# Optimization experiments

Hardware: AMD Instinct MI355X
Metric: run time of the kernel (lower is better)

The kernel has to match this reference:

```python
import jax, jax.numpy as jnp
import numpy as np
from jax.scipy.special import logsumexp

B, T, D, H, K = 32, 512, 768, 256, 32


def setup_inputs() -> dict:
    key = jax.random.key(0)
    ks = jax.random.split(key, 12)
    x = jax.random.normal(ks[0], (B, T, D), jnp.float32)
    lengths = jax.random.randint(ks[1], (B,), T // 2, T + 1).astype(jnp.int32)
    mask = jnp.arange(T)[None, :] < lengths[:, None]  # [B,T] bool
    targets = jax.random.randint(ks[2], (B, T), 0, K)

    def p(k, shape, fan):
        return jax.random.normal(k, shape, jnp.float32) / np.sqrt(fan).astype(np.float32)

    W_ih_f = p(ks[3], (4 * H, D), D); W_hh_f = p(ks[4], (4 * H, H), H)
    W_ih_b = p(ks[5], (4 * H, D), D); W_hh_b = p(ks[6], (4 * H, H), H)
    b_f = jnp.zeros((4 * H,), jnp.float32); b_b = jnp.zeros((4 * H,), jnp.float32)
    W_clf = p(ks[7], (K, 2 * H), 2 * H); b_clf = jnp.zeros((K,), jnp.float32)
    start_t = jax.random.uniform(ks[8], (K,), jnp.float32, -0.1, 0.1)
    end_t = jax.random.uniform(ks[9], (K,), jnp.float32, -0.1, 0.1)
    trans = jax.random.uniform(ks[10], (K, K), jnp.float32, -0.1, 0.1)
    return {"input": x, "lengths": lengths, "mask": mask, "targets": targets,
            "W_ih_f": W_ih_f, "W_hh_f": W_hh_f, "b_f": b_f,
            "W_ih_b": W_ih_b, "W_hh_b": W_hh_b, "b_b": b_b,
            "W_clf": W_clf, "b_clf": b_clf,
            "start_t": start_t, "end_t": end_t, "trans": trans}


def _lstm_dir(x_tbd, W_ih, W_hh, b):
    # x_tbd: [T,B,D] -> hs [T,B,H], torch gate order (i,f,g,o)
    Hh = W_hh.shape[1]
    pre = jnp.einsum('tbd,gd->tbg', x_tbd, W_ih) + b  # precompute input projections

    def step(carry, p_t):
        h, c = carry
        g = p_t + h @ W_hh.T
        i, f, gg, o = jnp.split(g, 4, axis=-1)
        c = jax.nn.sigmoid(f) * c + jax.nn.sigmoid(i) * jnp.tanh(gg)
        h = jax.nn.sigmoid(o) * jnp.tanh(c)
        return (h, c), h

    b_sz = x_tbd.shape[1]
    init = (jnp.zeros((b_sz, Hh), x_tbd.dtype), jnp.zeros((b_sz, Hh), x_tbd.dtype))
    _, hs = jax.lax.scan(step, init, pre)
    return hs


def _emissions(x, lengths, W_ih_f, W_hh_f, b_f, W_ih_b, W_hh_b, b_b, W_clf, b_clf):
    Tn = x.shape[1]
    t_idx = jnp.arange(Tn)[None, :]
    # per-sequence reversal of the valid prefix (emulates packed bidirectional LSTM)
    rev_idx = jnp.where(t_idx < lengths[:, None], lengths[:, None] - 1 - t_idx, t_idx)
    h_f = _lstm_dir(x.transpose(1, 0, 2), W_ih_f, W_hh_f, b_f).transpose(1, 0, 2)
    x_rev = jnp.take_along_axis(x, rev_idx[:, :, None], axis=1)
    h_b = _lstm_dir(x_rev.transpose(1, 0, 2), W_ih_b, W_hh_b, b_b).transpose(1, 0, 2)
    h_b = jnp.take_along_axis(h_b, rev_idx[:, :, None], axis=1)  # un-flip
    hcat = jnp.concatenate([h_f, h_b], axis=-1)  # [B,T,2H]
    return hcat @ W_clf.T + b_clf  # [B,T,K]


def _crf_nll(em, targets, mask, lengths, start_t, end_t, trans):
    maskf = mask.astype(em.dtype)
    # numerator (gold path score)
    em_sc = jnp.take_along_axis(em, targets[:, :, None], axis=2)[..., 0]  # [B,T]
    tr_sc = trans[targets[:, :-1], targets[:, 1:]]  # [B,T-1]
    num = start_t[targets[:, 0]] + em_sc[:, 0] + jnp.sum((tr_sc + em_sc[:, 1:]) * maskf[:, 1:], axis=1)
    last_tags = jnp.take_along_axis(targets, (lengths - 1).astype(targets.dtype)[:, None], axis=1)[:, 0]
    num = num + end_t[last_tags]
    # log partition via forward algorithm
    def fwd_step(alpha, inp):
        e_t, m_t = inp
        nxt = logsumexp(alpha[:, :, None] + trans[None] + e_t[:, None, :], axis=1)
        return jnp.where(m_t[:, None], nxt, alpha), None

    alpha0 = start_t[None] + em[:, 0]
    alpha, _ = jax.lax.scan(fwd_step, alpha0, (em[:, 1:].transpose(1, 0, 2), mask[:, 1:].T))
    logZ = logsumexp(alpha + end_t[None], axis=1)
    return -jnp.mean(num - logZ)


def _viterbi(em, mask, start_t, end_t, trans):
    Kn = trans.shape[0]

    def vit_step(score, inp):
        e_t, m_t = inp
        bc = score[:, :, None] + trans[None] + e_t[:, None, :]  # [B,Kprev,Kcur]
        nxt = jnp.max(bc, axis=1)
        idx = jnp.argmax(bc, axis=1)  # [B,K] best previous tag
        idx = jnp.where(m_t[:, None], idx, jnp.arange(Kn)[None, :])  # identity on pads
        return jnp.where(m_t[:, None], nxt, score), idx

    score0 = start_t[None] + em[:, 0]
    score, hist = jax.lax.scan(vit_step, score0, (em[:, 1:].transpose(1, 0, 2), mask[:, 1:].T))
    last = jnp.argmax(score + end_t[None], axis=1)  # [B]

    def back(tag, h):
        prev = jnp.take_along_axis(h, tag[:, None], axis=1)[:, 0]
        return prev, prev

    _, tags_prev = jax.lax.scan(back, last, hist, reverse=True)  # [T-1,B]
    tags = jnp.concatenate([tags_prev, last[None]], axis=0).T  # [B,T]
    return jnp.where(mask, tags, 0)  # zero_pad


def reference(input, lengths, mask, targets, W_ih_f, W_hh_f, b_f, W_ih_b, W_hh_b, b_b,
              W_clf, b_clf, start_t, end_t, trans):
    em = _emissions(input, lengths, W_ih_f, W_hh_f, b_f, W_ih_b, W_hh_b, b_b, W_clf, b_clf)
    loss = _crf_nll(em, targets, mask, lengths, start_t, end_t, trans)
    preds = _viterbi(em, mask, start_t, end_t, trans)
    return loss, preds
```

## Files before the change

### kernel.cpp

```cpp
#include <hip/hip_runtime.h>
#include <hip/hip_bf16.h>


#define NB 32
#define NT 512
#define ND 768
#define NH 256
#define NK 32

__global__ __launch_bounds__(256) void k_sgemm(const float* __restrict__ A,
                                               const float* __restrict__ Wf,
                                               const float* __restrict__ Wb,
                                               float* __restrict__ C) {
    __shared__ float As[2][16][132];
    __shared__ float Bs[2][16][132];
    const int tid = threadIdx.x;
    const int bx = blockIdx.x;
    const int by = blockIdx.y;
    const int tx = tid & 15, ty = tid >> 4;
    const int sm = tid >> 2;
    const int sk = (tid & 3) * 4;
    float acc[8][8];
#pragma unroll
    for (int i = 0; i < 8; ++i)
#pragma unroll
        for (int j = 0; j < 8; ++j) acc[i][j] = 0.f;

    const float* Arow0 = A + (size_t)(by * 128 + sm) * ND + sk;
    const float* Arow1 = A + (size_t)(by * 128 + 64 + sm) * ND + sk;
    const int gn0 = bx * 128 + sm, gn1 = gn0 + 64;
    const float* W0 = (gn0 < 1024) ? (Wf + (size_t)gn0 * ND + sk) : (Wb + (size_t)(gn0 - 1024) * ND + sk);
    const float* W1 = (gn1 < 1024) ? (Wf + (size_t)gn1 * ND + sk) : (Wb + (size_t)(gn1 - 1024) * ND + sk);

    {
        float4 a0 = *(const float4*)(Arow0);
        float4 a1 = *(const float4*)(Arow1);
        float4 w0 = *(const float4*)(W0);
        float4 w1 = *(const float4*)(W1);
        As[0][sk + 0][sm] = a0.x; As[0][sk + 1][sm] = a0.y; As[0][sk + 2][sm] = a0.z; As[0][sk + 3][sm] = a0.w;
        As[0][sk + 0][64 + sm] = a1.x; As[0][sk + 1][64 + sm] = a1.y; As[0][sk + 2][64 + sm] = a1.z; As[0][sk + 3][64 + sm] = a1.w;
        Bs[0][sk + 0][sm] = w0.x; Bs[0][sk + 1][sm] = w0.y; Bs[0][sk + 2][sm] = w0.z; Bs[0][sk + 3][sm] = w0.w;
        Bs[0][sk + 0][64 + sm] = w1.x; Bs[0][sk + 1][64 + sm] = w1.y; Bs[0][sk + 2][64 + sm] = w1.z; Bs[0][sk + 3][64 + sm] = w1.w;
    }
    __syncthreads();

    int cur = 0;
    for (int k0 = 0; k0 < ND; k0 += 16) {
        const bool more = (k0 + 16) < ND;
        float4 na0, na1, nw0, nw1;
        if (more) {
            na0 = *(const float4*)(Arow0 + k0 + 16);
            na1 = *(const float4*)(Arow1 + k0 + 16);
            nw0 = *(const float4*)(W0 + k0 + 16);
            nw1 = *(const float4*)(W1 + k0 + 16);
        }
#pragma unroll
        for (int kk = 0; kk < 16; ++kk) {
            float a[8], b[8];
            *(float4*)&a[0] = *(const float4*)&As[cur][kk][ty * 4];
            *(float4*)&a[4] = *(const float4*)&As[cur][kk][64 + ty * 4];
            *(float4*)&b[0] = *(const float4*)&Bs[cur][kk][tx * 4];
            *(float4*)&b[4] = *(const float4*)&Bs[cur][kk][64 + tx * 4];
#pragma unroll
            for (int i = 0; i < 8; ++i)
#pragma unroll
                for (int j = 0; j < 8; ++j)
                    acc[i][j] = fmaf(a[i], b[j], acc[i][j]);
        }
        if (more) {
            const int nxt = cur ^ 1;
            As[nxt][sk + 0][sm] = na0.x; As[nxt][sk + 1][sm] = na0.y; As[nxt][sk + 2][sm] = na0.z; As[nxt][sk + 3][sm] = na0.w;
            As[nxt][sk + 0][64 + sm] = na1.x; As[nxt][sk + 1][64 + sm] = na1.y; As[nxt][sk + 2][64 + sm] = na1.z; As[nxt][sk + 3][64 + sm] = na1.w;
            Bs[nxt][sk + 0][sm] = nw0.x; Bs[nxt][sk + 1][sm] = nw0.y; Bs[nxt][sk + 2][sm] = nw0.z; Bs[nxt][sk + 3][sm] = nw0.w;
            Bs[nxt][sk + 0][64 + sm] = nw1.x; Bs[nxt][sk + 1][64 + sm] = nw1.y; Bs[nxt][sk + 2][64 + sm] = nw1.z; Bs[nxt][sk + 3][64 + sm] = nw1.w;
            __syncthreads();
            cur = nxt;
        }
    }
#pragma unroll
    for (int i = 0; i < 8; ++i) {
        int m = by * 128 + ((i < 4) ? (ty * 4 + i) : (64 + ty * 4 + (i - 4)));
        float* Crow = C + (size_t)m * 2048 + bx * 128;
        *(float4*)(Crow + tx * 4)      = make_float4(acc[i][0], acc[i][1], acc[i][2], acc[i][3]);
        *(float4*)(Crow + 64 + tx * 4) = make_float4(acc[i][4], acc[i][5], acc[i][6], acc[i][7]);
    }
}

__global__ __launch_bounds__(256) void k_wt4(const float* __restrict__ Whf,
                                             const float* __restrict__ Whb,
                                             float4* __restrict__ Wt4) {
    int gid = blockIdx.x * 256 + threadIdx.x;
    if (gid >= 131072) return;
    int dir = gid >> 16;
    int k   = (gid >> 8) & 255;
    int j   = gid & 255;
    const float* W = dir ? Whb : Whf;
    Wt4[gid] = make_float4(W[(size_t)(0 * 256 + j) * 256 + k],
                           W[(size_t)(1 * 256 + j) * 256 + k],
                           W[(size_t)(2 * 256 + j) * 256 + k],
                           W[(size_t)(3 * 256 + j) * 256 + k]);
}

__device__ __forceinline__ float sigm(float x) { return 1.f / (1.f + expf(-x)); }

__global__ __launch_bounds__(256, 1) void k_lstm4(const float* __restrict__ C,
                                                  const float4* __restrict__ Wt4,
                                                  const float* __restrict__ b_f,
                                                  const float* __restrict__ b_b,
                                                  const int* __restrict__ lengths,
                                                  float* __restrict__ h_f,
                                                  float* __restrict__ h_b) {
    __shared__ float hsh[4][272];
    const int tid = threadIdx.x;
    const int g = blockIdx.x & 63, s = blockIdx.x >> 6;
    const int b = g & 31, dir = g >> 5;
    const int j0 = s * 64;
    const float* bias = dir ? b_b : b_f;
    float* hdir = dir ? h_b : h_f;

    const int j = tid >> 2;
    const int kq = tid & 3;
    const int w = tid >> 6;
    const int lane = tid & 63;

    float4 wreg[64];
    {
        const float4* wb = Wt4 + ((size_t)dir * 256 + kq * 64) * 256 + j0 + j;
#pragma unroll
        for (int i = 0; i < 64; ++i) wreg[i] = wb[(size_t)i * 256];
    }
    float4 breg = make_float4(0.f, 0.f, 0.f, 0.f);
    if (kq == 0)
        breg = make_float4(bias[j0 + j], bias[256 + j0 + j],
                           bias[512 + j0 + j], bias[768 + j0 + j]);
    const int mylen = lengths[b];
    float creg = 0.f;

    for (int t = 0; t < NT; ++t) {
        float4 pre = make_float4(0.f, 0.f, 0.f, 0.f);
        if (kq == 0) {
            int src_t = t;
            if (dir) src_t = (t < mylen) ? (mylen - 1 - t) : t;
            const float* Crow = C + (size_t)(b * 512 + src_t) * 2048 + dir * 1024 + j0 + j;
            pre.x = Crow[0]; pre.y = Crow[256]; pre.z = Crow[512]; pre.w = Crow[768];
        }
        float4 acc = make_float4(0.f, 0.f, 0.f, 0.f);
        if (t > 0) {
            const float* hp = hdir + ((size_t)b * 512 + (t - 1)) * 256 + 4 * lane;
            unsigned long long u0, u1;
            int guard = 0;
            for (;;) {
                u0 = __hip_atomic_load((const unsigned long long*)hp,
                                       __ATOMIC_RELAXED, __HIP_MEMORY_SCOPE_AGENT);
                u1 = __hip_atomic_load((const unsigned long long*)(hp + 2),
                                       __ATOMIC_RELAXED, __HIP_MEMORY_SCOPE_AGENT);
                if ((unsigned)(u0 & 0xFFFFFFFFu) != 0xFFFFFFFFu &&
                    (unsigned)(u0 >> 32)        != 0xFFFFFFFFu &&
                    (unsigned)(u1 & 0xFFFFFFFFu) != 0xFFFFFFFFu &&
                    (unsigned)(u1 >> 32)        != 0xFFFFFFFFu) break;
                if (++guard > (1 << 24)) break;
            }
            const int d0 = 4 * lane;
            float* dst = &hsh[w][(d0 >> 6) * 68 + (d0 & 63)];
            float lo0 = __uint_as_float((unsigned)(u0 & 0xFFFFFFFFu));
            float hi0 = __uint_as_float((unsigned)(u0 >> 32));
            float lo1 = __uint_as_float((unsigned)(u1 & 0xFFFFFFFFu));
            float hi1 = __uint_as_float((unsigned)(u1 >> 32));
            *(float4*)dst = make_float4(lo0, hi0, lo1, hi1);
            asm volatile("s_waitcnt lgkmcnt(0)" ::: "memory");
            __builtin_amdgcn_sched_barrier(0);
            const float* src = &hsh[w][kq * 68];
#pragma unroll
            for (int c = 0; c < 16; ++c) {
                float ha[4];
                *(float4*)ha = *(const float4*)(src + 4 * c);
#pragma unroll
                for (int i = 0; i < 4; ++i) {
                    float4 wv = wreg[c * 4 + i];
                    acc.x = fmaf(wv.x, ha[i], acc.x);
                    acc.y = fmaf(wv.y, ha[i], acc.y);
                    acc.z = fmaf(wv.z, ha[i], acc.z);
                    acc.w = fmaf(wv.w, ha[i], acc.w);
                }
            }
        }
        if (kq == 0) {
            acc.x += pre.x + breg.x; acc.y += pre.y + breg.y;
            acc.z += pre.z + breg.z; acc.w += pre.w + breg.w;
        }
#pragma unroll
        for (int off = 1; off <= 2; off <<= 1) {
            acc.x += __shfl_xor(acc.x, off);
            acc.y += __shfl_xor(acc.y, off);
            acc.z += __shfl_xor(acc.z, off);
            acc.w += __shfl_xor(acc.w, off);
        }
        float ig = sigm(acc.x), fg = sigm(acc.y), gt = tanhf(acc.z), og = sigm(acc.w);
        creg = fg * creg + ig * gt;
        float hn = og * tanhf(creg);
        if (kq == 0)
            __hip_atomic_store(hdir + ((size_t)b * 512 + t) * 256 + j0 + j, hn,
                               __ATOMIC_RELAXED, __HIP_MEMORY_SCOPE_AGENT);
    }
}

__global__ __launch_bounds__(256) void k_em(const float* __restrict__ hf,
                                            const float* __restrict__ hb,
                                            const float* __restrict__ Wclf,
                                            const float* __restrict__ bclf,
                                            const int* __restrict__ lengths,
                                            float* __restrict__ em) {
    extern __shared__ float4 wc4[];
    const int tid = threadIdx.x;
    for (int idx = tid; idx < 4096; idx += 256) {
        int jq = idx >> 5, ko = idx & 31;
        wc4[idx] = *(const float4*)(Wclf + (size_t)ko * 512 + jq * 4);
    }
    __syncthreads();
    const int r = tid >> 5, ko = tid & 31;
    const int m = blockIdx.x * 8 + r;
    const int b = m >> 9, t = m & 511;
    const int len = lengths[b];
    const int rev = (t < len) ? (len - 1 - t) : t;
    const float* hfr = hf + (size_t)m * 256;
    const float* hbr = hb + (size_t)(b * 512 + rev) * 256;
    float acc = bclf[ko];
#pragma unroll 4
    for (int jq = 0; jq < 64; ++jq) {
        float4 h4 = *(const float4*)(hfr + jq * 4);
        float4 ww = wc4[jq * 32 + ko];
        acc += h4.x * ww.x + h4.y * ww.y + h4.z * ww.z + h4.w * ww.w;
    }
#pragma unroll 4
    for (int jq = 0; jq < 64; ++jq) {
        float4 h4 = *(const float4*)(hbr + jq * 4);
        float4 ww = wc4[(64 + jq) * 32 + ko];
        acc += h4.x * ww.x + h4.y * ww.y + h4.z * ww.z + h4.w * ww.w;
    }
    em[(size_t)m * 32 + ko] = acc;
}

__global__ __launch_bounds__(64) void k_crfvit(const float* __restrict__ em,
                                               const int* __restrict__ targets,
                                               const int* __restrict__ lengths,
                                               const float* __restrict__ start_t,
                                               const float* __restrict__ end_t,
                                               const float* __restrict__ trans,
                                               float* __restrict__ numv,
                                               float* __restrict__ logZv,
                                               float* __restrict__ out) {
    __shared__ float trans_s[32][33];
    __shared__ float vec[32];
    __shared__ unsigned char hist[511 * 32];
    const int tid = threadIdx.x;
    const int b = blockIdx.x & 31;
    const int mode = blockIdx.x >> 5;
    for (int idx = tid; idx < 1024; idx += 64) trans_s[idx >> 5][idx & 31] = trans[idx];
    const int len = lengths[b];
    const float* emb = em + (size_t)b * 512 * 32;
    const int k = tid & 31, half = tid >> 5;
    if (tid < 32) vec[tid] = start_t[tid] + emb[tid];
    __syncthreads();

    if (mode == 0) {
        for (int t = 1; t < NT; ++t) {
            bool mv = t < len;
            int kp0 = half * 16;
            float m = -1e30f;
#pragma unroll 4
            for (int i = 0; i < 16; ++i)
                m = fmaxf(m, vec[kp0 + i] + trans_s[kp0 + i][k]);
            float m2 = fmaxf(m, __shfl_xor(m, 32));
            float ssum = 0.f;
#pragma unroll 4
            for (int i = 0; i < 16; ++i)
                ssum += __expf(vec[kp0 + i] + trans_s[kp0 + i][k] - m2);
            ssum += __shfl_xor(ssum, 32);
            float anew = m2 + __logf(ssum) + emb[t * 32 + k];
            __syncthreads();
            if (half == 0 && mv) vec[k] = anew;
            __syncthreads();
        }
        float val = (tid < 32) ? vec[tid] + end_t[tid] : -1e30f;
        float m = val;
#pragma unroll
        for (int off = 32; off >= 1; off >>= 1) m = fmaxf(m, __shfl_xor(m, off));
        float e = (tid < 32) ? __expf(val - m) : 0.f;
#pragma unroll
        for (int off = 32; off >= 1; off >>= 1) e += __shfl_xor(e, off);
        if (tid == 0) logZv[b] = m + __logf(e);
        const int* tg = targets + b * 512;
        float partial = 0.f;
        for (int t = 1 + tid; t < NT; t += 64) {
            if (t < len) {
                int y0 = tg[t - 1], y1 = tg[t];
                partial += trans_s[y0][y1] + emb[t * 32 + y1];
            }
        }
#pragma unroll
        for (int off = 32; off >= 1; off >>= 1) partial += __shfl_xor(partial, off);
        if (tid == 0) {
            int y00 = tg[0];
            int yl = tg[len - 1];
            numv[b] = partial + start_t[y00] + emb[y00] + end_t[yl];
        }
    } else {
        for (int t = 1; t < NT; ++t) {
            bool mv = t < len;
            int kp0 = half * 16;
            float e = emb[t * 32 + k];
            float m = -1e30f; int mi = kp0;
#pragma unroll 4
            for (int i = 0; i < 16; ++i) {
                float v = (vec[kp0 + i] + trans_s[kp0 + i][k]) + e;
                if (v > m) { m = v; mi = kp0 + i; }
            }
            float mo = __shfl_xor(m, 32);
            int io = __shfl_xor(mi, 32);
            float mlow = half ? mo : m;   int ilow = half ? io : mi;
            float mhigh = half ? m : mo;  int ihigh = half ? mi : io;
            float bm; int bi;
            if (mhigh > mlow) { bm = mhigh; bi = ihigh; } else { bm = mlow; bi = ilow; }
            __syncthreads();
            if (half == 0) {
                hist[(t - 1) * 32 + k] = (unsigned char)(mv ? bi : k);
                if (mv) vec[k] = bm;
            }
            __syncthreads();
        }
        float val = (tid < 32) ? vec[tid] + end_t[tid] : -1e30f;
        int idx = (tid < 32) ? tid : 63;
#pragma unroll
        for (int off = 32; off >= 1; off >>= 1) {
            float vo = __shfl_xor(val, off);
            int io = __shfl_xor(idx, off);
            if (vo > val || (vo == val && io < idx)) { val = vo; idx = io; }
        }
        int cur = idx;
        float* ob = out + 1 + (size_t)b * 512;
        if (tid == 0) ob[511] = (511 < len) ? (float)cur : 0.f;
        for (int t2 = 510; t2 >= 0; --t2) {
            cur = hist[t2 * 32 + cur];
            if (tid == 0) ob[t2] = (t2 < len) ? (float)cur : 0.f;
        }
    }
}

__global__ __launch_bounds__(64) void k_loss(const float* __restrict__ numv,
                                             const float* __restrict__ logZv,
                                             float* __restrict__ out) {
    int tid = threadIdx.x;
    float v = (tid < 32) ? (logZv[tid] - numv[tid]) : 0.f;
#pragma unroll
    for (int off = 32; off >= 1; off >>= 1) v += __shfl_xor(v, off);
    if (tid == 0) out[0] = v / 32.f;
}

extern "C" void kernel_launch(void* const* d_in, const int* in_sizes, int n_in,
                              void* d_out, int out_size, void* d_ws, size_t ws_size,
                              hipStream_t stream) {
    const float* x       = (const float*)d_in[0];
    const int*   lengths = (const int*)d_in[1];
    const int*   targets = (const int*)d_in[3];
    const float* W_ih_f  = (const float*)d_in[4];
    const float* W_hh_f  = (const float*)d_in[5];
    const float* b_f     = (const float*)d_in[6];
    const float* W_ih_b  = (const float*)d_in[7];
    const float* W_hh_b  = (const float*)d_in[8];
    const float* b_b     = (const float*)d_in[9];
    const float* W_clf   = (const float*)d_in[10];
    const float* b_clf   = (const float*)d_in[11];
    const float* start_t = (const float*)d_in[12];
    const float* end_t   = (const float*)d_in[13];
    const float* trans   = (const float*)d_in[14];
    float* out = (float*)d_out;
    float* ws = (float*)d_ws;

    float* C     = ws;
    float* h_f   = C + (size_t)16384 * 2048;
    float* h_b   = h_f + (size_t)32 * 512 * 256;
    float* em    = h_b + (size_t)32 * 512 * 256;
    float4* Wt4  = (float4*)(em + (size_t)32 * 512 * 32);
    float* numv  = (float*)(Wt4 + 131072);
    float* logZv = numv + 32;

    hipMemsetAsync(h_f, 0xFF, (size_t)2 * 32 * 512 * 256 * sizeof(float), stream);
    k_wt4<<<512, 256, 0, stream>>>(W_hh_f, W_hh_b, Wt4);
    k_sgemm<<<dim3(16, 128), 256, 0, stream>>>(x, W_ih_f, W_ih_b, C);
    k_lstm4<<<256, 256, 0, stream>>>(C, Wt4, b_f, b_b, lengths, h_f, h_b);
    k_em<<<2048, 256, 65536, stream>>>(h_f, h_b, W_clf, b_clf, lengths, em);
    k_crfvit<<<64, 64, 0, stream>>>(em, targets, lengths, start_t, end_t, trans, numv, logZv, out);
    k_loss<<<1, 64, 0, stream>>>(numv, logZv, out);
}
```

Before: 2.563 ms.

## Split LSTM recurrence across twice as many blocks with weights in registers and LDS

The recurrent LSTM kernel now uses 512 blocks, each owning 32 hidden units instead of 64. Each thread covers a 32-element slice of the hidden-state reduction, with half of its W_hh slice in registers and half in shared memory, so register pressure drops enough for two blocks per CU. The aim is to shorten each block's serial per-step dot product and spread the recurrence over more CUs. In exchange there are twice as many blocks spin-waiting on global hidden-state flags, an extra shuffle stage in the reduction, LDS weight reads on every step, and a hang risk if all 512 spinning blocks are not resident at once.

```diff
diff --git a/kernel.cpp b/kernel.cpp
--- a/kernel.cpp
+++ b/kernel.cpp
@@ -103,46 +103,46 @@
 
 __device__ __forceinline__ float sigm(float x) { return 1.f / (1.f + expf(-x)); }
 
-__global__ __launch_bounds__(256, 1) void k_lstm4(const float* __restrict__ C,
+__global__ __launch_bounds__(256, 2) void k_lstm5(const float* __restrict__ C,
                                                   const float4* __restrict__ Wt4,
                                                   const float* __restrict__ b_f,
                                                   const float* __restrict__ b_b,
                                                   const int* __restrict__ lengths,
                                                   float* __restrict__ h_f,
                                                   float* __restrict__ h_b) {
-    __shared__ float hsh[4][272];
+    __shared__ float4 wlds[16][256];
+    __shared__ float hsh[4][288];
     const int tid = threadIdx.x;
     const int g = blockIdx.x & 63, s = blockIdx.x >> 6;
     const int b = g & 31, dir = g >> 5;
-    const int j0 = s * 64;
+    const int j0 = s * 32;
     const float* bias = dir ? b_b : b_f;
     float* hdir = dir ? h_b : h_f;
 
-    const int j = tid >> 2;
-    const int kq = tid & 3;
+    const int j = tid >> 3;
+    const int kq = tid & 7;
     const int w = tid >> 6;
     const int lane = tid & 63;
 
-    float4 wreg[64];
+    float4 wreg[16];
     {
-        const float4* wb = Wt4 + ((size_t)dir * 256 + kq * 64) * 256 + j0 + j;
-#pragma unroll
-        for (int i = 0; i < 64; ++i) wreg[i] = wb[(size_t)i * 256];
-    }
-    float4 breg = make_float4(0.f, 0.f, 0.f, 0.f);
-    if (kq == 0)
-        breg = make_float4(bias[j0 + j], bias[256 + j0 + j],
-                           bias[512 + j0 + j], bias[768 + j0 + j]);
+        const float4* wb = Wt4 + ((size_t)dir * 256 + 32 * kq) * 256 + j0 + j;
+#pragma unroll
+        for (int u = 0; u < 16; ++u) wreg[u] = wb[(size_t)u * 256];
+#pragma unroll
+        for (int u = 0; u < 16; ++u) wlds[u][tid] = wb[(size_t)(16 + u) * 256];
+    }
+    float preBias = (kq < 4) ? bias[kq * 256 + j0 + j] : 0.f;
     const int mylen = lengths[b];
     float creg = 0.f;
+    __syncthreads();
 
     for (int t = 0; t < NT; ++t) {
-        float4 pre = make_float4(0.f, 0.f, 0.f, 0.f);
-        if (kq == 0) {
+        float preS = 0.f;
+        if (kq < 4) {
             int src_t = t;
             if (dir) src_t = (t < mylen) ? (mylen - 1 - t) : t;
-            const float* Crow = C + (size_t)(b * 512 + src_t) * 2048 + dir * 1024 + j0 + j;
-            pre.x = Crow[0]; pre.y = Crow[256]; pre.z = Crow[512]; pre.w = Crow[768];
+            preS = C[(size_t)(b * 512 + src_t) * 2048 + dir * 1024 + kq * 256 + j0 + j];
         }
         float4 acc = make_float4(0.f, 0.f, 0.f, 0.f);
         if (t > 0) {
@@ -158,22 +158,21 @@
                     (unsigned)(u0 >> 32)        != 0xFFFFFFFFu &&
                     (unsigned)(u1 & 0xFFFFFFFFu) != 0xFFFFFFFFu &&
                     (unsigned)(u1 >> 32)        != 0xFFFFFFFFu) break;
-                if (++guard > (1 << 24)) break;
-            }
-            const int d0 = 4 * lane;
-            float* dst = &hsh[w][(d0 >> 6) * 68 + (d0 & 63)];
-            float lo0 = __uint_as_float((unsigned)(u0 & 0xFFFFFFFFu));
-            float hi0 = __uint_as_float((unsigned)(u0 >> 32));
-            float lo1 = __uint_as_float((unsigned)(u1 & 0xFFFFFFFFu));
-            float hi1 = __uint_as_float((unsigned)(u1 >> 32));
-            *(float4*)dst = make_float4(lo0, hi0, lo1, hi1);
+                if (++guard > (1 << 22)) break;
+            }
+            float* dst = &hsh[w][(lane >> 3) * 36 + ((4 * lane) & 31)];
+            *(float4*)dst = make_float4(
+                __uint_as_float((unsigned)(u0 & 0xFFFFFFFFu)),
+                __uint_as_float((unsigned)(u0 >> 32)),
+                __uint_as_float((unsigned)(u1 & 0xFFFFFFFFu)),
+                __uint_as_float((unsigned)(u1 >> 32)));
             asm volatile("s_waitcnt lgkmcnt(0)" ::: "memory");
             __builtin_amdgcn_sched_barrier(0);
-            const float* src = &hsh[w][kq * 68];
-#pragma unroll
-            for (int c = 0; c < 16; ++c) {
+            const float* hbp = &hsh[w][kq * 36];
+#pragma unroll
+            for (int c = 0; c < 4; ++c) {
                 float ha[4];
-                *(float4*)ha = *(const float4*)(src + 4 * c);
+                *(float4*)ha = *(const float4*)(hbp + 4 * c);
 #pragma unroll
                 for (int i = 0; i < 4; ++i) {
                     float4 wv = wreg[c * 4 + i];
@@ -183,13 +182,27 @@
                     acc.w = fmaf(wv.w, ha[i], acc.w);
                 }
             }
-        }
-        if (kq == 0) {
-            acc.x += pre.x + breg.x; acc.y += pre.y + breg.y;
-            acc.z += pre.z + breg.z; acc.w += pre.w + breg.w;
-        }
-#pragma unroll
-        for (int off = 1; off <= 2; off <<= 1) {
+#pragma unroll
+            for (int c = 0; c < 4; ++c) {
+                float ha[4];
+                *(float4*)ha = *(const float4*)(hbp + 16 + 4 * c);
+#pragma unroll
+                for (int i = 0; i < 4; ++i) {
+                    float4 wv = wlds[c * 4 + i][tid];
+                    acc.x = fmaf(wv.x, ha[i], acc.x);
+                    acc.y = fmaf(wv.y, ha[i], acc.y);
+                    acc.z = fmaf(wv.z, ha[i], acc.z);
+                    acc.w = fmaf(wv.w, ha[i], acc.w);
+                }
+            }
+        }
+        float add = preS + preBias;
+        acc.x += (kq == 0) ? add : 0.f;
+        acc.y += (kq == 1) ? add : 0.f;
+        acc.z += (kq == 2) ? add : 0.f;
+        acc.w += (kq == 3) ? add : 0.f;
+#pragma unroll
+        for (int off = 1; off <= 4; off <<= 1) {
             acc.x += __shfl_xor(acc.x, off);
             acc.y += __shfl_xor(acc.y, off);
             acc.z += __shfl_xor(acc.z, off);
@@ -387,7 +400,7 @@
     hipMemsetAsync(h_f, 0xFF, (size_t)2 * 32 * 512 * 256 * sizeof(float), stream);
     k_wt4<<<512, 256, 0, stream>>>(W_hh_f, W_hh_b, Wt4);
     k_sgemm<<<dim3(16, 128), 256, 0, stream>>>(x, W_ih_f, W_ih_b, C);
-    k_lstm4<<<256, 256, 0, stream>>>(C, Wt4, b_f, b_b, lengths, h_f, h_b);
+    k_lstm5<<<512, 256, 0, stream>>>(C, Wt4, b_f, b_b, lengths, h_f, h_b);
     k_em<<<2048, 256, 65536, stream>>>(h_f, h_b, W_clf, b_clf, lengths, em);
     k_crfvit<<<64, 64, 0, stream>>>(em, targets, lengths, start_t, end_t, trans, numv, logZv, out);
     k_loss<<<1, 64, 0, stream>>>(numv, logZv, out);
```

Result: slower. 3.256 ms (+27.1%).
